# Performance work log

Measured on AMD Instinct MI355X. Metric: run time of the kernel, lower is better.

Reference implementation:

```python
import jax, jax.numpy as jnp
import numpy as np

B, S, D, H, FF = 2, 2048, 1024, 16, 4096
DH = D // H
EPS = 1e-5


def rmsnorm(x, g):
    rms = jnp.sqrt(jnp.mean(x * x, axis=-1, keepdims=True) + EPS)
    return x / rms * g


def gelu(x):
    return x * 0.5 * (1.0 + jax.lax.erf(x / np.float32(np.sqrt(2.0))))


def setup_inputs() -> dict:
    key = jax.random.key(0)
    ks = jax.random.split(key, 9)
    sd = np.float32(1.0 / np.sqrt(D))
    sf = np.float32(1.0 / np.sqrt(FF))
    return {
        'x': jax.random.normal(ks[0], (B, S, D), jnp.float32),
        'wq': jax.random.normal(ks[1], (D, D), jnp.float32) * sd,
        'wk': jax.random.normal(ks[2], (D, D), jnp.float32) * sd,
        'wv': jax.random.normal(ks[3], (D, D), jnp.float32) * sd,
        'wo': jax.random.normal(ks[4], (D, D), jnp.float32) * sd,
        'w1': jax.random.normal(ks[5], (FF, D), jnp.float32) * sd,
        'w2': jax.random.normal(ks[6], (D, FF), jnp.float32) * sf,
        'g1': jax.random.uniform(ks[7], (D,), jnp.float32),
        'g2': jax.random.uniform(ks[8], (D,), jnp.float32),
    }


def reference(x, wq, wk, wv, wo, w1, w2, g1, g2):
    b, s, d = x.shape
    h = rmsnorm(x, g1)
    # torch Linear: y = x @ W.T ; split heads -> [b, s, H, DH]
    q = jnp.einsum('bsd,ed->bse', h, wq).reshape(b, s, H, DH)
    k = jnp.einsum('bsd,ed->bse', h, wk).reshape(b, s, H, DH)
    v = jnp.einsum('bsd,ed->bse', h, wv).reshape(b, s, H, DH)
    score = jnp.einsum('bqhd,bkhd->bhqk', q, k) / np.float32(np.sqrt(DH))
    causal = jnp.triu(jnp.ones((s, s), bool), 1)  # strictly upper = masked
    score = score + jnp.where(causal, jnp.float32(-1e9), jnp.float32(0.0))
    attn_w = jax.nn.softmax(score, axis=-1)
    o = jnp.einsum('bhqk,bkhd->bqhd', attn_w, v).reshape(b, s, d)
    attn_out = jnp.einsum('bsd,ed->bse', o, wo)
    x2 = attn_out + x
    h2 = rmsnorm(x2, g2)
    ffn = jnp.einsum('bsf,df->bsd', gelu(jnp.einsum('bsd,fd->bsf', h2, w1)), w2)
    return ffn + x2
```

## Files before the change

kernel.cpp:

```cpp
#include <hip/hip_runtime.h>
#include <cstdint>

#define B_ 2
#define S_ 2048
#define D_ 1024
#define H_ 16
#define DH_ 64
#define FF_ 4096
#define M_TOK (B_ * S_)

typedef __attribute__((ext_vector_type(8))) short short8;
typedef __attribute__((ext_vector_type(4))) float f32x4;
typedef __attribute__((ext_vector_type(4))) unsigned short us4;

typedef unsigned short u16;

#define SCL 0.18033688011112042f

__device__ __forceinline__ float bf2f(u16 u) {
  union { uint32_t u; float f; } x;
  x.u = ((uint32_t)u) << 16;
  return x.f;
}
__device__ __forceinline__ u16 f2bf(float f) {
  union { float f; uint32_t u; } x;
  x.f = f;
  uint32_t r = x.u + 0x7FFFu + ((x.u >> 16) & 1u);
  return (u16)(r >> 16);
}

__device__ __forceinline__ uint32_t pack2bf(float a, float b) {
  union { float f; uint32_t u; } x, y;
  x.f = a; y.f = b;
#if __has_builtin(__builtin_amdgcn_perm)
  return __builtin_amdgcn_perm(y.u + 0x8000u, x.u + 0x8000u, 0x07060302u);
#else
  return ((x.u + 0x8000u) >> 16) | ((y.u + 0x8000u) & 0xFFFF0000u);
#endif
}

__device__ __forceinline__ void gl_lds16(const void* g, void* l) {
  __builtin_amdgcn_global_load_lds(
      (const __attribute__((address_space(1))) uint32_t*)(uintptr_t)g,
      (__attribute__((address_space(3))) uint32_t*)(uintptr_t)l, 16, 0, 0);
}

__device__ __forceinline__ float gelu_f(float v) {
  const float y = 0.7978845608f * (v + 0.044715f * v * v * v);
  const float t = exp2f(y * 2.885390082f);
  const float th = 1.0f - 2.0f * __builtin_amdgcn_rcpf(t + 1.0f);
  return 0.5f * v * (1.0f + th);
}

#define MEG 1048576
#define PREP_CVT 12288
#define PREP_ZERO 4160

__global__ __launch_bounds__(256) void prep_k(const float* __restrict__ wq, const float* __restrict__ wk,
                                              const float* __restrict__ wv, const float* __restrict__ wo,
                                              const float* __restrict__ w1, const float* __restrict__ w2,
                                              u16* __restrict__ wqkv, u16* __restrict__ wob,
                                              u16* __restrict__ w1b, u16* __restrict__ w2b,
                                              float* __restrict__ Of, float* __restrict__ L,
                                              const float* __restrict__ X, const float* __restrict__ G,
                                              u16* __restrict__ Hout) {
  __shared__ float red[4];
  const int bid = blockIdx.x;
  const int tid = threadIdx.x;
  if (bid < PREP_CVT) {
    const int n = (bid * 256 + tid) * 4;
    const float* src;
    u16* dst;
    int off;
    if (n < 3 * MEG) {
      dst = wqkv; off = n;
      src = (n < MEG) ? wq + n : (n < 2 * MEG ? wk + (n - MEG) : wv + (n - 2 * MEG));
    } else if (n < 4 * MEG) {
      dst = wob; off = n - 3 * MEG; src = wo + off;
    } else if (n < 8 * MEG) {
      dst = w1b; off = n - 4 * MEG; src = w1 + off;
    } else {
      dst = w2b; off = n - 8 * MEG; src = w2 + off;
    }
    const float4 v = *(const float4*)src;
    us4 o;
    o[0] = f2bf(v.x); o[1] = f2bf(v.y); o[2] = f2bf(v.z); o[3] = f2bf(v.w);
    *(us4*)&dst[off] = o;
  } else if (bid < PREP_CVT + PREP_ZERO) {
    const int i = ((bid - PREP_CVT) * 256 + tid) * 4;
    if (i < 4 * MEG) { *(float4*)&Of[i] = float4{0.f, 0.f, 0.f, 0.f}; }
    else { *(float4*)&L[i - 4 * MEG] = float4{0.f, 0.f, 0.f, 0.f}; }
  } else {
    const int row = bid - (PREP_CVT + PREP_ZERO);
    const float4 xx = *(const float4*)&X[(size_t)row * D_ + tid * 4];
    float v[4] = {xx.x, xx.y, xx.z, xx.w};
    float s = 0.f;
#pragma unroll
    for (int i = 0; i < 4; ++i) s += v[i] * v[i];
#pragma unroll
    for (int d = 1; d < 64; d <<= 1) s += __shfl_xor(s, d);
    if ((tid & 63) == 0) red[tid >> 6] = s;
    __syncthreads();
    s = red[0] + red[1] + red[2] + red[3];
    const float scale = rsqrtf(s * (1.0f / (float)D_) + 1e-5f);
    const float4 gg = *(const float4*)&G[tid * 4];
    us4 o;
    o[0] = f2bf(v[0] * scale * gg.x);
    o[1] = f2bf(v[1] * scale * gg.y);
    o[2] = f2bf(v[2] * scale * gg.z);
    o[3] = f2bf(v[3] * scale * gg.w);
    *(us4*)&Hout[(size_t)row * D_ + tid * 4] = o;
  }
}

__global__ __launch_bounds__(256) void norm_o_k(const float* __restrict__ Of, const float* __restrict__ L,
                                                u16* __restrict__ O) {
  const int row = blockIdx.x;
  const int tid = threadIdx.x;
  const int col = tid * 4;
  const int hh = col >> 6;
  const float lv = L[(size_t)((row >> 11) * 16 + hh) * 2048 + (row & 2047)];
  const float inv = 1.0f / lv;
  const float4 v = *(const float4*)&Of[(size_t)row * D_ + col];
  us4 o;
  o[0] = f2bf(v.x * inv); o[1] = f2bf(v.y * inv);
  o[2] = f2bf(v.z * inv); o[3] = f2bf(v.w * inv);
  *(us4*)&O[(size_t)row * D_ + col] = o;
}

__global__ __launch_bounds__(256) void rmsnorm_wo_k(const u16* __restrict__ P0, const u16* __restrict__ P1,
                                                    const float* __restrict__ X, const float* __restrict__ G,
                                                    float* __restrict__ X2, u16* __restrict__ Hout) {
  const int row = blockIdx.x;
  const int tid = threadIdx.x;
  const size_t off = (size_t)row * D_ + tid * 4;
  const us4 p0 = *(const us4*)&P0[off];
  const us4 p1 = *(const us4*)&P1[off];
  const float4 xx = *(const float4*)&X[off];
  float v[4];
  v[0] = bf2f(p0[0]) + bf2f(p1[0]) + xx.x;
  v[1] = bf2f(p0[1]) + bf2f(p1[1]) + xx.y;
  v[2] = bf2f(p0[2]) + bf2f(p1[2]) + xx.z;
  v[3] = bf2f(p0[3]) + bf2f(p1[3]) + xx.w;
  *(float4*)&X2[off] = float4{v[0], v[1], v[2], v[3]};
  float s = 0.f;
#pragma unroll
  for (int i = 0; i < 4; ++i) s += v[i] * v[i];
#pragma unroll
  for (int d = 1; d < 64; d <<= 1) s += __shfl_xor(s, d);
  __shared__ float red[4];
  if ((tid & 63) == 0) red[tid >> 6] = s;
  __syncthreads();
  s = red[0] + red[1] + red[2] + red[3];
  const float scale = rsqrtf(s * (1.0f / (float)D_) + 1e-5f);
  const float4 gg = *(const float4*)&G[tid * 4];
  us4 o;
  o[0] = f2bf(v[0] * scale * gg.x);
  o[1] = f2bf(v[1] * scale * gg.y);
  o[2] = f2bf(v[2] * scale * gg.z);
  o[3] = f2bf(v[3] * scale * gg.w);
  *(us4*)&Hout[off] = o;
}

__global__ __launch_bounds__(256) void ffn2_red_k(const u16* __restrict__ Q0, const u16* __restrict__ Q1,
                                                  float* __restrict__ OUT) {
  const int i = (blockIdx.x * 256 + threadIdx.x) * 4;
  const us4 a = *(const us4*)&Q0[i];
  const us4 b = *(const us4*)&Q1[i];
  const float4 c = *(const float4*)&OUT[i];
  *(float4*)&OUT[i] = float4{bf2f(a[0]) + bf2f(b[0]) + c.x, bf2f(a[1]) + bf2f(b[1]) + c.y,
                             bf2f(a[2]) + bf2f(b[2]) + c.z, bf2f(a[3]) + bf2f(b[3]) + c.w};
}

template <int MODE>
__global__ __launch_bounds__(256) void gemm_bt_k(const u16* __restrict__ A,
                                                 const u16* __restrict__ W,
                                                 u16* __restrict__ C0, u16* __restrict__ C1,
                                                 u16* __restrict__ C2, int N, int K) {
  __shared__ alignas(16) u16 As[256 * 32];
  __shared__ alignas(16) u16 Bs[256 * 32];
  const int tid = threadIdx.x;
  const int wv = tid >> 6, lane = tid & 63;
  const int r = lane & 15, quad = lane >> 4;
  const int nx = gridDim.x;
  const int nwg = nx * gridDim.y;
  const int orig = blockIdx.x + nx * blockIdx.y;
  const int id = (orig & 7) * (nwg >> 3) + (orig >> 3);
  const int bn = (id % nx) * 128;
  const int bm = (id / nx) * 128;
  const int row0 = (wv >> 1) * 64, col0 = (wv & 1) * 64;

  f32x4 acc[4][4] = {};

  int sm[4], sh[4], sg[4];
#pragma unroll
  for (int jj = 0; jj < 4; ++jj) {
    const int c = wv * 256 + jj * 64 + lane;
    const int lr = c >> 2;
    sm[jj] = lr & 127;
    sh[jj] = lr >> 7;
    sg[jj] = (c & 3) ^ ((sm[jj] >> 1) & 3);
  }

  for (int k0 = 0; k0 < K; k0 += 64) {
#pragma unroll
    for (int jj = 0; jj < 4; ++jj) {
      const int l0 = (wv * 256 + jj * 64) * 8;
      gl_lds16(&A[(size_t)(bm + sm[jj]) * K + k0 + sh[jj] * 32 + sg[jj] * 8], &As[l0]);
      gl_lds16(&W[(size_t)(bn + sm[jj]) * K + k0 + sh[jj] * 32 + sg[jj] * 8], &Bs[l0]);
    }
    __syncthreads();
#pragma unroll
    for (int h = 0; h < 2; ++h) {
      short8 af[4], bf[4];
#pragma unroll
      for (int mt = 0; mt < 4; ++mt) {
        const int mr = row0 + mt * 16 + r;
        af[mt] = *(const short8*)&As[(mr + 128 * h) * 32 + (quad ^ ((mr >> 1) & 3)) * 8];
      }
#pragma unroll
      for (int nt = 0; nt < 4; ++nt) {
        const int nr = col0 + nt * 16 + r;
        bf[nt] = *(const short8*)&Bs[(nr + 128 * h) * 32 + (quad ^ ((nr >> 1) & 3)) * 8];
      }
#pragma unroll
      for (int mt = 0; mt < 4; ++mt)
#pragma unroll
        for (int nt = 0; nt < 4; ++nt)
          acc[mt][nt] = __builtin_amdgcn_mfma_f32_16x16x32_bf16(af[mt], bf[nt], acc[mt][nt], 0, 0, 0);
    }
    __syncthreads();
  }

  if constexpr (MODE == 2) {
#pragma unroll
    for (int mt = 0; mt < 4; ++mt)
#pragma unroll
      for (int nt = 0; nt < 4; ++nt)
#pragma unroll
        for (int i = 0; i < 4; ++i) {
          const int grow = bm + row0 + mt * 16 + quad * 4 + i;
          const int gcol = bn + col0 + nt * 16 + r;
          C0[(size_t)grow * N + gcol] = f2bf(gelu_f(acc[mt][nt][i]));
        }
  } else {
    if (bn < 2048) {
#pragma unroll
      for (int mt = 0; mt < 4; ++mt) {
        const int grow0 = bm + row0 + mt * 16 + quad * 4;
#pragma unroll
        for (int nt = 0; nt < 4; ++nt) {
          const int gcol = bn + col0 + nt * 16 + r;
          u16* dst = (gcol < 1024) ? C0 : C1;
          const float sc = (gcol < 1024) ? SCL : 1.0f;
          const int cc = gcol & 1023;
#pragma unroll
          for (int i = 0; i < 4; ++i)
            dst[(size_t)(grow0 + i) * 1024 + cc] = f2bf(acc[mt][nt][i] * sc);
        }
      }
    } else {
#pragma unroll
      for (int mtp = 0; mtp < 4; mtp += 2) {
        const int tok0 = bm + row0 + mtp * 16 + quad * 4;
#pragma unroll
        for (int nt = 0; nt < 4; ++nt) {
          const int vcol = bn + col0 + nt * 16 + r - 2048;
          const size_t vtrow = (size_t)((tok0 >> 11) * 16 + (vcol >> 6)) * 64 + (vcol & 63);
#pragma unroll
          for (int i = 0; i < 4; ++i) {
            const int s = (tok0 + i) & 2047;
            const uint32_t pk =
                (uint32_t)f2bf(acc[mtp][nt][i]) | ((uint32_t)f2bf(acc[mtp + 1][nt][i]) << 16);
            *(uint32_t*)&C2[vtrow * 2048 + s + (s & 15)] = pk;
          }
        }
      }
    }
  }
}

__global__ __launch_bounds__(256) void gemm_sk2_k(const u16* __restrict__ A,
                                                  const u16* __restrict__ W,
                                                  u16* __restrict__ P0, u16* __restrict__ P1,
                                                  int N, int K, int KS) {
  __shared__ alignas(16) u16 As[256 * 32];
  __shared__ alignas(16) u16 Bs[256 * 32];
  const int tid = threadIdx.x;
  const int wv = tid >> 6, lane = tid & 63;
  const int r = lane & 15, quad = lane >> 4;
  const int orig = blockIdx.x + 8 * (blockIdx.y + 32 * blockIdx.z);
  const int id = (orig & 7) * 64 + (orig >> 3);
  const int bn = (id & 7) * 128;
  const int bm = ((id >> 3) & 31) * 128;
  const int bz = id >> 8;
  const int row0 = (wv >> 1) * 64, col0 = (wv & 1) * 64;
  const int koff = bz * KS;
  u16* P = bz ? P1 : P0;

  f32x4 acc[4][4] = {};

  int sm[4], sh[4], sg[4];
#pragma unroll
  for (int jj = 0; jj < 4; ++jj) {
    const int c = wv * 256 + jj * 64 + lane;
    const int lr = c >> 2;
    sm[jj] = lr & 127;
    sh[jj] = lr >> 7;
    sg[jj] = (c & 3) ^ ((sm[jj] >> 1) & 3);
  }

  for (int k0 = koff; k0 < koff + KS; k0 += 64) {
#pragma unroll
    for (int jj = 0; jj < 4; ++jj) {
      const int l0 = (wv * 256 + jj * 64) * 8;
      gl_lds16(&A[(size_t)(bm + sm[jj]) * K + k0 + sh[jj] * 32 + sg[jj] * 8], &As[l0]);
      gl_lds16(&W[(size_t)(bn + sm[jj]) * K + k0 + sh[jj] * 32 + sg[jj] * 8], &Bs[l0]);
    }
    __syncthreads();
#pragma unroll
    for (int h = 0; h < 2; ++h) {
      short8 af[4], bf[4];
#pragma unroll
      for (int mt = 0; mt < 4; ++mt) {
        const int mr = row0 + mt * 16 + r;
        af[mt] = *(const short8*)&As[(mr + 128 * h) * 32 + (quad ^ ((mr >> 1) & 3)) * 8];
      }
#pragma unroll
      for (int nt = 0; nt < 4; ++nt) {
        const int nr = col0 + nt * 16 + r;
        bf[nt] = *(const short8*)&Bs[(nr + 128 * h) * 32 + (quad ^ ((nr >> 1) & 3)) * 8];
      }
#pragma unroll
      for (int mt = 0; mt < 4; ++mt)
#pragma unroll
        for (int nt = 0; nt < 4; ++nt)
          acc[mt][nt] = __builtin_amdgcn_mfma_f32_16x16x32_bf16(af[mt], bf[nt], acc[mt][nt], 0, 0, 0);
    }
    __syncthreads();
  }

#pragma unroll
  for (int mt = 0; mt < 4; ++mt)
#pragma unroll
    for (int nt = 0; nt < 4; ++nt)
#pragma unroll
      for (int i = 0; i < 4; ++i) {
        const int grow = bm + row0 + mt * 16 + quad * 4 + i;
        const int gcol = bn + col0 + nt * 16 + r;
        P[(size_t)grow * N + gcol] = f2bf(acc[mt][nt][i]);
      }
}

#define ATTN_BODY(BUF, J0, RINK, RINV, ROUTK, ROUTV, DO_PF, DO_WR)                                 \
  {                                                                                                \
    __syncthreads();                                                                               \
    if (DO_PF) {                                                                                   \
      ROUTK = *(const short8*)&Kb[(size_t)((J0) + 64 + krow) * D_ + kg * 8];                       \
      ROUTV = *(const short8*)&VTb[(size_t)vrow * 2048 + (J0) + 64 + vg * 8];                      \
    }                                                                                              \
    f32x4 z[2][2];                                                                                 \
    __builtin_amdgcn_s_setprio(1);                                                                 \
    _Pragma("unroll") for (int kt = 0; kt < 2; ++kt) {                                             \
      const short8 kf0 = *(const short8*)&Ks[BUF][(kt * 16 + r) * 72 + quad * 8];                  \
      const short8 kf1 = *(const short8*)&Ks[BUF][(kt * 16 + r) * 72 + 32 + quad * 8];             \
      _Pragma("unroll") for (int f = 0; f < 2; ++f) {                                              \
        f32x4 zz = {};                                                                             \
        zz = __builtin_amdgcn_mfma_f32_16x16x32_bf16(qf[f][0], kf0, zz, 0, 0, 0);                  \
        zz = __builtin_amdgcn_mfma_f32_16x16x32_bf16(qf[f][1], kf1, zz, 0, 0, 0);                  \
        z[f][kt] = zz;                                                                             \
      }                                                                                            \
    }                                                                                              \
    __builtin_amdgcn_s_setprio(0);                                                                 \
    const bool masked = ((J0) + 31 > m0);                                                          \
    _Pragma("unroll") for (int f = 0; f < 2; ++f) _Pragma("unroll") for (int i = 0; i < 4; ++i) {  \
      const int qrow = m0 + f * 16 + quad * 4 + i;                                                 \
      float v0 = z[f][0][i];                                                                       \
      float v1 = z[f][1][i];                                                                       \
      if (masked) {                                                                                \
        if ((J0) + r > qrow) v0 = -128.f;                                                          \
        if ((J0) + 16 + r > qrow) v1 = -128.f;                                                     \
      }                                                                                            \
      *(uint32_t*)&Psw[(f * 16 + quad * 4 + i) * 40 + r * 2] = pack2bf(exp2f(v0), exp2f(v1));      \
    }                                                                                              \
    asm volatile("s_waitcnt lgkmcnt(0)" ::: "memory");                                             \
    short8 vf[4];                                                                                  \
    _Pragma("unroll") for (int nt = 0; nt < 4; ++nt)                                               \
        vf[nt] = *(const short8*)&Vs[BUF][(nt * 16 + r) * 40 + quad * 8];                          \
    __builtin_amdgcn_s_setprio(1);                                                                 \
    _Pragma("unroll") for (int f = 0; f < 2; ++f) {                                                \
      const short8 pf = *(const short8*)&Psw[(f * 16 + r) * 40 + quad * 8];                        \
      _Pragma("unroll") for (int nt = 0; nt < 4; ++nt)                                             \
          oacc[f][nt] = __builtin_amdgcn_mfma_f32_16x16x32_bf16(pf, vf[nt], oacc[f][nt], 0, 0, 0); \
      lacc[f] = __builtin_amdgcn_mfma_f32_16x16x32_bf16(pf, onesv, lacc[f], 0, 0, 0);              \
    }                                                                                              \
    __builtin_amdgcn_s_setprio(0);                                                                 \
    if (DO_WR) {                                                                                   \
      *(short8*)&Ks[(BUF) ^ 1][krow * 72 + kg * 8] = RINK;                                         \
      *(short8*)&Vs[(BUF) ^ 1][vrow * 40 + vg * 8] = RINV;                                         \
    }                                                                                              \
  }

__global__ __launch_bounds__(256, 2) void attn_k(const u16* __restrict__ Q,
                                                 const u16* __restrict__ Kx,
                                                 const u16* __restrict__ VT,
                                                 float* __restrict__ Of, float* __restrict__ L) {
  __shared__ alignas(16) u16 Ks[2][32 * 72];
  __shared__ alignas(16) u16 Vs[2][64 * 40];
  __shared__ alignas(16) u16 Ps[4][32 * 40];

  const int tid = threadIdx.x;
  const int wv = tid >> 6, lane = tid & 63;
  const int r = lane & 15, quad = lane >> 4;

  const int orig = blockIdx.x + 40 * blockIdx.y;
  const int sid = (orig & 7) * 160 + (orig >> 3);
  const int sx = sid % 40;
  const int bh = sid / 40;
  const int b = bh >> 4, hh = bh & 15;

  int id = 39 - sx;
  int bx = 0;
  for (;;) {
    const int nb = (bx >> 2) + 1;
    if (id < nb) break;
    id -= nb;
    ++bx;
  }
  const int c = id;
  const int j0base = c * 512;
  const int niter = (min(bx * 128 + 128, j0base + 512) - j0base) >> 5;

  const int qbase = bx * 128;
  const int m0 = qbase + wv * 32;
  const size_t base = (size_t)b * S_ * D_ + (size_t)hh * DH_;
  const u16* Qb = Q + base;
  const u16* Kb = Kx + base;
  const u16* VTb = VT + (size_t)bh * 64 * 2048;
  u16* Psw = &Ps[wv][0];

  short8 qf[2][2];
#pragma unroll
  for (int f = 0; f < 2; ++f) {
    qf[f][0] = *(const short8*)&Qb[(size_t)(m0 + f * 16 + r) * D_ + quad * 8];
    qf[f][1] = *(const short8*)&Qb[(size_t)(m0 + f * 16 + r) * D_ + 32 + quad * 8];
  }

  short8 onesv;
#pragma unroll
  for (int e = 0; e < 8; ++e) onesv[e] = (short)0x3F80;

  f32x4 oacc[2][4] = {};
  f32x4 lacc[2] = {};

  const int krow = tid >> 3, kg = tid & 7;
  const int vrow = tid >> 2, vg = tid & 3;

  *(short8*)&Ks[0][krow * 72 + kg * 8] = *(const short8*)&Kb[(size_t)(j0base + krow) * D_ + kg * 8];
  *(short8*)&Vs[0][vrow * 40 + vg * 8] = *(const short8*)&VTb[(size_t)vrow * 2048 + j0base + vg * 8];
  short8 kA, vA, kB, vB;
  kA = *(const short8*)&Kb[(size_t)(j0base + 32 + krow) * D_ + kg * 8];
  vA = *(const short8*)&VTb[(size_t)vrow * 2048 + j0base + 32 + vg * 8];

  for (int it = 0; it < niter; it += 2) {
    const int j0 = j0base + it * 32;
    ATTN_BODY(0, j0, kA, vA, kB, vB, (it + 2 < niter), true);
    ATTN_BODY(1, j0 + 32, kB, vB, kA, vA, (it + 3 < niter), (it + 2 < niter));
  }

#pragma unroll
  for (int f = 0; f < 2; ++f) {
#pragma unroll
    for (int i = 0; i < 4; ++i) {
      const int qrow = m0 + f * 16 + quad * 4 + i;
#pragma unroll
      for (int nt = 0; nt < 4; ++nt)
        atomicAdd(&Of[base + (size_t)qrow * D_ + nt * 16 + r], oacc[f][nt][i]);
      if (r == 0) atomicAdd(&L[(size_t)bh * 2048 + qrow], lacc[f][i]);
    }
  }
}

extern "C" void kernel_launch(void* const* d_in, const int* in_sizes, int n_in,
                              void* d_out, int out_size, void* d_ws, size_t ws_size,
                              hipStream_t stream) {
  (void)in_sizes; (void)n_in; (void)out_size; (void)ws_size;
  const float* x   = (const float*)d_in[0];
  const float* wq  = (const float*)d_in[1];
  const float* wk  = (const float*)d_in[2];
  const float* wvp = (const float*)d_in[3];
  const float* wo  = (const float*)d_in[4];
  const float* w1  = (const float*)d_in[5];
  const float* w2  = (const float*)d_in[6];
  const float* g1  = (const float*)d_in[7];
  const float* g2  = (const float*)d_in[8];
  float* out = (float*)d_out;

  u16* ws = (u16*)d_ws;
  const size_t TD = (size_t)M_TOK * D_;
  u16* h    = ws;
  u16* q    = ws + 1 * TD;
  u16* k    = ws + 2 * TD;
  u16* vt   = ws + 3 * TD;
  u16* h2   = ws + 4 * TD;
  float* l  = (float*)(ws + 4 * TD);
  u16* o    = h;
  u16* t    = ws;
  u16* P0   = q;
  u16* P1   = k;
  u16* Q0   = h2;
  u16* wqkv = ws + 5 * TD;
  u16* wob  = wqkv + 3 * MEG;
  u16* w1b  = wob + 1 * MEG;
  u16* w2b  = w1b + 4 * MEG;
  u16* Q1   = w2b + 4 * MEG;

  const dim3 blk(256);

  prep_k<<<PREP_CVT + PREP_ZERO + M_TOK, blk, 0, stream>>>(wq, wk, wvp, wo, w1, w2, wqkv, wob,
                                                           w1b, w2b, out, l, x, g1, h);
  gemm_bt_k<4><<<dim3(24, 32), blk, 0, stream>>>(h, wqkv, q, k, vt, 3072, 1024);
  attn_k<<<dim3(40, 32), blk, 0, stream>>>(q, k, vt, out, l);
  norm_o_k<<<M_TOK, blk, 0, stream>>>(out, l, o);
  gemm_sk2_k<<<dim3(8, 32, 2), blk, 0, stream>>>(o, wob, P0, P1, 1024, 1024, 512);
  rmsnorm_wo_k<<<M_TOK, blk, 0, stream>>>(P0, P1, x, g2, out, h2);
  gemm_bt_k<2><<<dim3(32, 32), blk, 0, stream>>>(h2, w1b, t, nullptr, nullptr, 4096, 1024);
  gemm_sk2_k<<<dim3(8, 32, 2), blk, 0, stream>>>(t, w2b, Q0, Q1, 1024, 4096, 2048);
  ffn2_red_k<<<4096, blk, 0, stream>>>(Q0, Q1, out);
}
```

Measured before the change: 348.6 us.

## Drop split-KV attention atomics; normalize and write bf16 output in-kernel

Attention no longer splits the key range into 512-wide chunks accumulated with float atomics. Each block now handles one 128-row query tile over its full causal key range and divides by the row sum before writing bf16 directly. This removes the zeroing pass in prep, the separate normalization kernel and the atomic traffic. Blocks are interleaved so heavy and light query tiles are paired, but there are now fewer blocks (512 instead of 1280) with unequal work, which risks a long tail and lower occupancy.

```diff
diff --git a/kernel.cpp b/kernel.cpp
--- a/kernel.cpp
+++ b/kernel.cpp
@@ -54,14 +54,12 @@
 
 #define MEG 1048576
 #define PREP_CVT 12288
-#define PREP_ZERO 4160
 
 __global__ __launch_bounds__(256) void prep_k(const float* __restrict__ wq, const float* __restrict__ wk,
                                               const float* __restrict__ wv, const float* __restrict__ wo,
                                               const float* __restrict__ w1, const float* __restrict__ w2,
                                               u16* __restrict__ wqkv, u16* __restrict__ wob,
                                               u16* __restrict__ w1b, u16* __restrict__ w2b,
-                                              float* __restrict__ Of, float* __restrict__ L,
                                               const float* __restrict__ X, const float* __restrict__ G,
                                               u16* __restrict__ Hout) {
   __shared__ float red[4];
@@ -86,12 +84,8 @@
     us4 o;
     o[0] = f2bf(v.x); o[1] = f2bf(v.y); o[2] = f2bf(v.z); o[3] = f2bf(v.w);
     *(us4*)&dst[off] = o;
-  } else if (bid < PREP_CVT + PREP_ZERO) {
-    const int i = ((bid - PREP_CVT) * 256 + tid) * 4;
-    if (i < 4 * MEG) { *(float4*)&Of[i] = float4{0.f, 0.f, 0.f, 0.f}; }
-    else { *(float4*)&L[i - 4 * MEG] = float4{0.f, 0.f, 0.f, 0.f}; }
   } else {
-    const int row = bid - (PREP_CVT + PREP_ZERO);
+    const int row = bid - PREP_CVT;
     const float4 xx = *(const float4*)&X[(size_t)row * D_ + tid * 4];
     float v[4] = {xx.x, xx.y, xx.z, xx.w};
     float s = 0.f;
@@ -111,21 +105,6 @@
     o[3] = f2bf(v[3] * scale * gg.w);
     *(us4*)&Hout[(size_t)row * D_ + tid * 4] = o;
   }
-}
-
-__global__ __launch_bounds__(256) void norm_o_k(const float* __restrict__ Of, const float* __restrict__ L,
-                                                u16* __restrict__ O) {
-  const int row = blockIdx.x;
-  const int tid = threadIdx.x;
-  const int col = tid * 4;
-  const int hh = col >> 6;
-  const float lv = L[(size_t)((row >> 11) * 16 + hh) * 2048 + (row & 2047)];
-  const float inv = 1.0f / lv;
-  const float4 v = *(const float4*)&Of[(size_t)row * D_ + col];
-  us4 o;
-  o[0] = f2bf(v.x * inv); o[1] = f2bf(v.y * inv);
-  o[2] = f2bf(v.z * inv); o[3] = f2bf(v.w * inv);
-  *(us4*)&O[(size_t)row * D_ + col] = o;
 }
 
 __global__ __launch_bounds__(256) void rmsnorm_wo_k(const u16* __restrict__ P0, const u16* __restrict__ P1,
@@ -404,7 +383,7 @@
 __global__ __launch_bounds__(256, 2) void attn_k(const u16* __restrict__ Q,
                                                  const u16* __restrict__ Kx,
                                                  const u16* __restrict__ VT,
-                                                 float* __restrict__ Of, float* __restrict__ L) {
+                                                 u16* __restrict__ O) {
   __shared__ alignas(16) u16 Ks[2][32 * 72];
   __shared__ alignas(16) u16 Vs[2][64 * 40];
   __shared__ alignas(16) u16 Ps[4][32 * 40];
@@ -413,26 +392,15 @@
   const int wv = tid >> 6, lane = tid & 63;
   const int r = lane & 15, quad = lane >> 4;
 
-  const int orig = blockIdx.x + 40 * blockIdx.y;
-  const int sid = (orig & 7) * 160 + (orig >> 3);
-  const int sx = sid % 40;
-  const int bh = sid / 40;
+  const int orig = blockIdx.x + 16 * blockIdx.y;
+  const int sid = (orig & 7) * 64 + (orig >> 3);
+  const int bh = sid >> 4;
+  const int t = sid & 15;
+  const int bx = (t & 1) ? (15 - (t >> 1)) : (t >> 1);
   const int b = bh >> 4, hh = bh & 15;
 
-  int id = 39 - sx;
-  int bx = 0;
-  for (;;) {
-    const int nb = (bx >> 2) + 1;
-    if (id < nb) break;
-    id -= nb;
-    ++bx;
-  }
-  const int c = id;
-  const int j0base = c * 512;
-  const int niter = (min(bx * 128 + 128, j0base + 512) - j0base) >> 5;
-
-  const int qbase = bx * 128;
-  const int m0 = qbase + wv * 32;
+  const int niter = (bx + 1) * 4;
+  const int m0 = bx * 128 + wv * 32;
   const size_t base = (size_t)b * S_ * D_ + (size_t)hh * DH_;
   const u16* Qb = Q + base;
   const u16* Kb = Kx + base;
@@ -456,14 +424,14 @@
   const int krow = tid >> 3, kg = tid & 7;
   const int vrow = tid >> 2, vg = tid & 3;
 
-  *(short8*)&Ks[0][krow * 72 + kg * 8] = *(const short8*)&Kb[(size_t)(j0base + krow) * D_ + kg * 8];
-  *(short8*)&Vs[0][vrow * 40 + vg * 8] = *(const short8*)&VTb[(size_t)vrow * 2048 + j0base + vg * 8];
+  *(short8*)&Ks[0][krow * 72 + kg * 8] = *(const short8*)&Kb[(size_t)krow * D_ + kg * 8];
+  *(short8*)&Vs[0][vrow * 40 + vg * 8] = *(const short8*)&VTb[(size_t)vrow * 2048 + vg * 8];
   short8 kA, vA, kB, vB;
-  kA = *(const short8*)&Kb[(size_t)(j0base + 32 + krow) * D_ + kg * 8];
-  vA = *(const short8*)&VTb[(size_t)vrow * 2048 + j0base + 32 + vg * 8];
+  kA = *(const short8*)&Kb[(size_t)(32 + krow) * D_ + kg * 8];
+  vA = *(const short8*)&VTb[(size_t)vrow * 2048 + 32 + vg * 8];
 
   for (int it = 0; it < niter; it += 2) {
-    const int j0 = j0base + it * 32;
+    const int j0 = it * 32;
     ATTN_BODY(0, j0, kA, vA, kB, vB, (it + 2 < niter), true);
     ATTN_BODY(1, j0 + 32, kB, vB, kA, vA, (it + 3 < niter), (it + 2 < niter));
   }
@@ -473,10 +441,10 @@
 #pragma unroll
     for (int i = 0; i < 4; ++i) {
       const int qrow = m0 + f * 16 + quad * 4 + i;
+      const float linv = 1.0f / lacc[f][i];
 #pragma unroll
       for (int nt = 0; nt < 4; ++nt)
-        atomicAdd(&Of[base + (size_t)qrow * D_ + nt * 16 + r], oacc[f][nt][i]);
-      if (r == 0) atomicAdd(&L[(size_t)bh * 2048 + qrow], lacc[f][i]);
+        O[base + (size_t)qrow * D_ + nt * 16 + r] = f2bf(oacc[f][nt][i] * linv);
     }
   }
 }
@@ -503,7 +471,6 @@
   u16* k    = ws + 2 * TD;
   u16* vt   = ws + 3 * TD;
   u16* h2   = ws + 4 * TD;
-  float* l  = (float*)(ws + 4 * TD);
   u16* o    = h;
   u16* t    = ws;
   u16* P0   = q;
@@ -517,11 +484,10 @@
 
   const dim3 blk(256);
 
-  prep_k<<<PREP_CVT + PREP_ZERO + M_TOK, blk, 0, stream>>>(wq, wk, wvp, wo, w1, w2, wqkv, wob,
-                                                           w1b, w2b, out, l, x, g1, h);
+  prep_k<<<PREP_CVT + M_TOK, blk, 0, stream>>>(wq, wk, wvp, wo, w1, w2, wqkv, wob, w1b, w2b,
+                                               x, g1, h);
   gemm_bt_k<4><<<dim3(24, 32), blk, 0, stream>>>(h, wqkv, q, k, vt, 3072, 1024);
-  attn_k<<<dim3(40, 32), blk, 0, stream>>>(q, k, vt, out, l);
-  norm_o_k<<<M_TOK, blk, 0, stream>>>(out, l, o);
+  attn_k<<<dim3(16, 32), blk, 0, stream>>>(q, k, vt, o);
   gemm_sk2_k<<<dim3(8, 32, 2), blk, 0, stream>>>(o, wob, P0, P1, 1024, 1024, 512);
   rmsnorm_wo_k<<<M_TOK, blk, 0, stream>>>(P0, P1, x, g2, out, h2);
   gemm_bt_k<2><<<dim3(32, 32), blk, 0, stream>>>(h2, w1b, t, nullptr, nullptr, 4096, 1024);
```

Measured after the change: 357.5 us. +2.5%, slower.
